# Kernel tuning notes

Measured on AMD Instinct MI355X. Metric: run time of the kernel, lower is better.

## Reference

```python
import jax, jax.numpy as jnp
import numpy as np

T = 524288          # 2**19 hash table size per level (power of 2)
F = 2               # features per table entry
NL = [16, 22, 30, 42, 58, 80, 111, 153, 212, 293, 406, 561, 775, 1071, 1481, 2046]
L_DIR = 4           # direction positional encoding freqs: 3 + 2*4*3 = 27
AABB = 3.0
PI1, PI2, PI3 = 1, 2654435761, 805459861
N_PTS = 1000000

_BITS = np.array([[(v >> k) & 1 for k in range(3)] for v in range(8)], dtype=bool)  # [8,3] corner offsets


def _linear(key, fan_in, fan_out):
    lim = 1.0 / np.sqrt(fan_in)
    kw, kb = jax.random.split(key)
    W = jax.random.uniform(kw, (fan_in, fan_out), jnp.float32, -lim, lim)
    b = jax.random.uniform(kb, (fan_out,), jnp.float32, -lim, lim)
    return W, b


def setup_inputs() -> dict:
    key = jax.random.key(0)
    ks = jax.random.split(key, 8)
    x = jax.random.normal(ks[0], (N_PTS, 3), jnp.float32)   # world-space sample points
    d = jax.random.normal(ks[1], (N_PTS, 3), jnp.float32)   # view directions
    tables = (jax.random.uniform(ks[2], (len(NL), T, F), jnp.float32) * 2 - 1) * 1e-4
    dW1, db1 = _linear(ks[3], F * len(NL), 64)
    dW2, db2 = _linear(ks[4], 64, 16)
    cW1, cb1 = _linear(ks[5], 27 + 16, 64)
    cW2, cb2 = _linear(ks[6], 64, 64)
    cW3, cb3 = _linear(ks[7], 64, 3)
    return dict(x=x, d=d, tables=tables, dW1=dW1, db1=db1, dW2=dW2, db2=db2,
                cW1=cW1, cb1=cb1, cW2=cW2, cb2=cb2, cW3=cW3, cb3=cb3)


def _hash_encode(xs, tables):
    # xs: [n,3] in [0,1]^3. Multi-resolution hash grid + trilinear interpolation.
    bits = jnp.asarray(_BITS)  # [8,3] bool
    feats = []
    for i, n in enumerate(NL):
        xn = xs * n
        fl = jnp.floor(xn)
        w = xn - fl                                   # [n,3] trilinear weights
        fl_i = fl.astype(jnp.uint32)
        ce_i = jnp.ceil(xn).astype(jnp.uint32)
        corner = jnp.where(bits[None], ce_i[:, None, :], fl_i[:, None, :])   # [n,8,3]
        # spatial hash: xor of coord * prime, mod T; T is 2**19 so uint32
        # wraparound multiply is exact mod T (bit-mask)
        h = ((corner[..., 0] * jnp.uint32(PI1))
             ^ (corner[..., 1] * jnp.uint32(PI2))
             ^ (corner[..., 2] * jnp.uint32(PI3))) & jnp.uint32(T - 1)       # [n,8]
        vals = tables[i][h]                            # [n,8,F] irregular gather
        wc = jnp.prod(jnp.where(bits[None], w[:, None, :], 1.0 - w[:, None, :]), axis=-1)  # [n,8]
        feats.append(jnp.einsum('nv,nvf->nf', wc, vals))
    return jnp.concatenate(feats, axis=1)              # [n, F*len(NL)] = [n,32]


def _pos_enc(d):
    outs = [d]
    for i in range(L_DIR):
        outs.append(jnp.sin((2.0 ** i) * d))
        outs.append(jnp.cos((2.0 ** i) * d))
    return jnp.concatenate(outs, axis=1)               # [n,27]


def reference(x, d, tables, dW1, db1, dW2, db2, cW1, cb1, cW2, cb2, cW3, cb3):
    xs = x / AABB
    mask = (jnp.abs(xs[:, 0]) < 0.5) & (jnp.abs(xs[:, 1]) < 0.5) & (jnp.abs(xs[:, 2]) < 0.5)
    xs = jnp.clip(xs + 0.5, 0.0, 1.0)                  # out-of-box rows get masked below
    feats = _hash_encode(xs, tables)
    h = jnp.maximum(feats @ dW1 + db1, 0.0) @ dW2 + db2            # [n,16] density MLP
    c_in = jnp.concatenate([h, _pos_enc(d)], axis=1)               # [n,43]
    hid = jnp.maximum(c_in @ cW1 + cb1, 0.0)
    hid = jnp.maximum(hid @ cW2 + cb2, 0.0)
    col = jax.nn.sigmoid(hid @ cW3 + cb3)                          # [n,3]
    color = jnp.where(mask[:, None], col, 0.0)
    log_sigma = jnp.where(mask, h[:, 0], -10000.0)
    return color, jnp.exp(log_sigma)
```

## Files before the change

kernel.cpp:

```cpp
#include <hip/hip_runtime.h>
#include <hip/hip_bf16.h>
#include <stdint.h>

#define TS 524288u
#define TMASK (TS - 1u)
#define QTOTAL 331757
#define NHL 11

typedef __attribute__((ext_vector_type(8))) short bf16x8;
typedef __attribute__((ext_vector_type(4))) float f32x4;

__device__ __forceinline__ short f2bf(float f) {
    union { float f; uint32_t u; } v; v.f = f;
    const uint32_t r = (v.u + 0x7fffu + ((v.u >> 16) & 1u)) >> 16;
    return (short)r;
}
__device__ __forceinline__ uint32_t cvtpk(float a, float b) {
    uint32_t r;
    asm("v_cvt_pk_bf16_f32 %0, %1, %2" : "=v"(r) : "v"(a), "v"(b));
    return r;
}
__device__ __forceinline__ short bf1(float a) { return (short)(cvtpk(a, a) & 0xffffu); }
__device__ __forceinline__ float bflo(uint32_t u) { return __uint_as_float(u << 16); }
__device__ __forceinline__ float bfhi(uint32_t u) { return __uint_as_float(u & 0xffff0000u); }
__device__ __forceinline__ uint32_t pack2(float a, float b) {
    return (uint32_t)(uint16_t)f2bf(a) | ((uint32_t)(uint16_t)f2bf(b) << 16);
}

__constant__ float c_NLf[16] = {16.f,22.f,30.f,42.f,58.f,80.f,111.f,153.f,
                                212.f,293.f,406.f,561.f,775.f,1071.f,1481.f,2046.f};
__constant__ int c_NP1[5]  = {17, 23, 31, 43, 59};
__constant__ int c_QOFF[5] = {0, 4913, 17080, 46871, 126378};

__global__ __launch_bounds__(256)
void cvt_tables_h(const float2* __restrict__ src, uint32_t* __restrict__ dst, int npairs)
{
    const int i = blockIdx.x * 256 + threadIdx.x;
    if (i >= npairs) return;
    const float2 v = src[i];
    dst[i] = pack2(v.x, v.y);
}

__global__ __launch_bounds__(256)
void build_quad(const float2* __restrict__ tbf, uint4* __restrict__ quad)
{
    const int i = blockIdx.x * 256 + threadIdx.x;
    if (i >= QTOTAL) return;
    int l, base;
    if      (i <   4913) { l = 0; base = 0;      }
    else if (i <  17080) { l = 1; base = 4913;   }
    else if (i <  46871) { l = 2; base = 17080;  }
    else if (i < 126378) { l = 3; base = 46871;  }
    else                 { l = 4; base = 126378; }
    const int np1 = c_NP1[l];
    int r = i - base;
    const int z = r % np1; r /= np1;
    const int y = r % np1;
    const int x = r / np1;
    const float2* tb = tbf + (size_t)l * TS;
    const uint32_t hx  = (uint32_t)x;
    const uint32_t hy0 = (uint32_t)y       * 2654435761u;
    const uint32_t hy1 = (uint32_t)(y + 1) * 2654435761u;
    const uint32_t hz0 = (uint32_t)z       * 805459861u;
    const uint32_t hz1 = (uint32_t)(z + 1) * 805459861u;
    const float2 a = tb[(hx ^ hy0 ^ hz0) & TMASK];
    const float2 b = tb[(hx ^ hy0 ^ hz1) & TMASK];
    const float2 c = tb[(hx ^ hy1 ^ hz0) & TMASK];
    const float2 d = tb[(hx ^ hy1 ^ hz1) & TMASK];
    uint4 q;
    q.x = pack2(a.x, a.y);
    q.y = pack2(b.x, b.y);
    q.z = pack2(c.x, c.y);
    q.w = pack2(d.x, d.y);
    quad[i] = q;
}

__device__ __forceinline__ uint32_t enc_pt(const int l, const float sx, const float sy,
                                           const float sz,
                                           const uint32_t* __restrict__ tb16h,
                                           const uint4* __restrict__ qtab)
{
    const float nf = c_NLf[l];
    const float xn0 = sx * nf, xn1 = sy * nf, xn2 = sz * nf;
    const float fl0 = floorf(xn0), fl1 = floorf(xn1), fl2 = floorf(xn2);
    const float w0 = xn0 - fl0, w1 = xn1 - fl1, w2 = xn2 - fl2;
    const uint32_t f0 = (uint32_t)fl0, f1 = (uint32_t)fl1, f2 = (uint32_t)fl2;

    float v0x,v0y,v1x,v1y,v2x,v2y,v3x,v3y,v4x,v4y,v5x,v5y,v6x,v6y,v7x,v7y;

    if (l < 5) {
        const int np1 = c_NP1[l];
        const uint4* qt = qtab + c_QOFF[l];
        const int cell = ((int)f0 * np1 + (int)f1) * np1 + (int)f2;
        const uint4 qa = qt[cell];
        const uint4 qb = qt[cell + np1 * np1];
        v0x = bflo(qa.x); v0y = bfhi(qa.x);
        v4x = bflo(qa.y); v4y = bfhi(qa.y);
        v2x = bflo(qa.z); v2y = bfhi(qa.z);
        v6x = bflo(qa.w); v6y = bfhi(qa.w);
        v1x = bflo(qb.x); v1y = bfhi(qb.x);
        v5x = bflo(qb.y); v5y = bfhi(qb.y);
        v3x = bflo(qb.z); v3y = bfhi(qb.z);
        v7x = bflo(qb.w); v7y = bfhi(qb.w);
    } else {
        const uint32_t c0 = (uint32_t)ceilf(xn0);
        const uint32_t c1 = (uint32_t)ceilf(xn1);
        const uint32_t c2 = (uint32_t)ceilf(xn2);
        const uint32_t hyf = f1 * 2654435761u, hyc = c1 * 2654435761u;
        const uint32_t hzf = f2 * 805459861u,  hzc = c2 * 805459861u;
        const uint32_t* tb = tb16h + (size_t)(l - 5) * TS;
        const uint32_t Sff = hyf ^ hzf, Scf = hyc ^ hzf;
        const uint32_t Sfc = hyf ^ hzc, Scc = hyc ^ hzc;
        uint32_t e0,e1,e2,e3,e4,e5,e6,e7;
        if ((f0 ^ c0) == 1u) {
            const uint32_t h0 = (f0 ^ Sff) & TMASK;
            const uint32_t h2 = (f0 ^ Scf) & TMASK;
            const uint32_t h4 = (f0 ^ Sfc) & TMASK;
            const uint32_t h6 = (f0 ^ Scc) & TMASK;
            const uint2 t0 = *reinterpret_cast<const uint2*>(tb + (h0 & ~1u));
            const uint2 t2 = *reinterpret_cast<const uint2*>(tb + (h2 & ~1u));
            const uint2 t4 = *reinterpret_cast<const uint2*>(tb + (h4 & ~1u));
            const uint2 t6 = *reinterpret_cast<const uint2*>(tb + (h6 & ~1u));
            e0 = (h0 & 1u) ? t0.y : t0.x;  e1 = (h0 & 1u) ? t0.x : t0.y;
            e2 = (h2 & 1u) ? t2.y : t2.x;  e3 = (h2 & 1u) ? t2.x : t2.y;
            e4 = (h4 & 1u) ? t4.y : t4.x;  e5 = (h4 & 1u) ? t4.x : t4.y;
            e6 = (h6 & 1u) ? t6.y : t6.x;  e7 = (h6 & 1u) ? t6.x : t6.y;
        } else {
            e0 = tb[(f0 ^ Sff) & TMASK];  e1 = tb[(c0 ^ Sff) & TMASK];
            e2 = tb[(f0 ^ Scf) & TMASK];  e3 = tb[(c0 ^ Scf) & TMASK];
            e4 = tb[(f0 ^ Sfc) & TMASK];  e5 = tb[(c0 ^ Sfc) & TMASK];
            e6 = tb[(f0 ^ Scc) & TMASK];  e7 = tb[(c0 ^ Scc) & TMASK];
        }
        v0x = bflo(e0); v0y = bfhi(e0); v1x = bflo(e1); v1y = bfhi(e1);
        v2x = bflo(e2); v2y = bfhi(e2); v3x = bflo(e3); v3y = bfhi(e3);
        v4x = bflo(e4); v4y = bfhi(e4); v5x = bflo(e5); v5y = bfhi(e5);
        v6x = bflo(e6); v6y = bfhi(e6); v7x = bflo(e7); v7y = bfhi(e7);
    }

    const float u0 = 1.0f - w0, u1 = 1.0f - w1, u2 = 1.0f - w2;
    float a0, a1;
    a0 = u0*u1*u2 * v0x;              a1 = u0*u1*u2 * v0y;
    a0 = fmaf(w0*u1*u2, v1x, a0);     a1 = fmaf(w0*u1*u2, v1y, a1);
    a0 = fmaf(u0*w1*u2, v2x, a0);     a1 = fmaf(u0*w1*u2, v2y, a1);
    a0 = fmaf(w0*w1*u2, v3x, a0);     a1 = fmaf(w0*w1*u2, v3y, a1);
    a0 = fmaf(u0*u1*w2, v4x, a0);     a1 = fmaf(u0*u1*w2, v4y, a1);
    a0 = fmaf(w0*u1*w2, v5x, a0);     a1 = fmaf(w0*u1*w2, v5y, a1);
    a0 = fmaf(u0*w1*w2, v6x, a0);     a1 = fmaf(u0*w1*w2, v6y, a1);
    a0 = fmaf(w0*w1*w2, v7x, a0);     a1 = fmaf(w0*w1*w2, v7y, a1);

    return cvtpk(a0, a1);
}

__global__ __launch_bounds__(256)
void ngp_encode_lm(const float* __restrict__ xg, const uint32_t* __restrict__ tb16h,
                   const uint4* __restrict__ qtab, uint32_t* __restrict__ feats_lm,
                   const int n, const unsigned tiles)
{
    const unsigned b = blockIdx.x;
    const int l = (int)(b / tiles);
    const int p = (int)(b - (unsigned)l * tiles) * 256 + threadIdx.x;
    if (p >= n) return;

    float sx = xg[3*p+0] / 3.0f, sy = xg[3*p+1] / 3.0f, sz = xg[3*p+2] / 3.0f;
    if (!((fabsf(sx) < 0.5f) && (fabsf(sy) < 0.5f) && (fabsf(sz) < 0.5f))) {
        feats_lm[(size_t)l * n + p] = 0u;
        return;
    }
    sx = fminf(fmaxf(sx + 0.5f, 0.0f), 1.0f);
    sy = fminf(fmaxf(sy + 0.5f, 0.0f), 1.0f);
    sz = fminf(fmaxf(sz + 0.5f, 0.0f), 1.0f);
    feats_lm[(size_t)l * n + p] = enc_pt(l, sx, sy, sz, tb16h, qtab);
}

__global__ __launch_bounds__(256)
void ngp_encode_f32(const float* __restrict__ xg, const float2* __restrict__ tbf,
                    uint32_t* __restrict__ feats_lm, const int n, const unsigned tiles)
{
    const unsigned b = blockIdx.x;
    const int l = (int)(b / tiles);
    const int p = (int)(b - (unsigned)l * tiles) * 256 + threadIdx.x;
    if (p >= n) return;
    float sx = xg[3*p+0] / 3.0f, sy = xg[3*p+1] / 3.0f, sz = xg[3*p+2] / 3.0f;
    if (!((fabsf(sx) < 0.5f) && (fabsf(sy) < 0.5f) && (fabsf(sz) < 0.5f))) {
        feats_lm[(size_t)l * n + p] = 0u;
        return;
    }
    sx = fminf(fmaxf(sx + 0.5f, 0.0f), 1.0f);
    sy = fminf(fmaxf(sy + 0.5f, 0.0f), 1.0f);
    sz = fminf(fmaxf(sz + 0.5f, 0.0f), 1.0f);
    const float nf = c_NLf[l];
    const float xn0 = sx*nf, xn1 = sy*nf, xn2 = sz*nf;
    const float fl0 = floorf(xn0), fl1 = floorf(xn1), fl2 = floorf(xn2);
    const float w0 = xn0-fl0, w1 = xn1-fl1, w2 = xn2-fl2;
    const uint32_t f0=(uint32_t)fl0, f1=(uint32_t)fl1, f2=(uint32_t)fl2;
    const uint32_t c0=(uint32_t)ceilf(xn0), c1=(uint32_t)ceilf(xn1), c2=(uint32_t)ceilf(xn2);
    const uint32_t hyf = f1*2654435761u, hyc = c1*2654435761u;
    const uint32_t hzf = f2*805459861u,  hzc = c2*805459861u;
    const float2* tb = tbf + (size_t)l * TS;
    const float2 e0 = tb[(f0^hyf^hzf)&TMASK], e1 = tb[(c0^hyf^hzf)&TMASK];
    const float2 e2 = tb[(f0^hyc^hzf)&TMASK], e3 = tb[(c0^hyc^hzf)&TMASK];
    const float2 e4 = tb[(f0^hyf^hzc)&TMASK], e5 = tb[(c0^hyf^hzc)&TMASK];
    const float2 e6 = tb[(f0^hyc^hzc)&TMASK], e7 = tb[(c0^hyc^hzc)&TMASK];
    const float u0 = 1.0f-w0, u1 = 1.0f-w1, u2 = 1.0f-w2;
    float a0, a1;
    a0 = u0*u1*u2 * e0.x;             a1 = u0*u1*u2 * e0.y;
    a0 = fmaf(w0*u1*u2, e1.x, a0);    a1 = fmaf(w0*u1*u2, e1.y, a1);
    a0 = fmaf(u0*w1*u2, e2.x, a0);    a1 = fmaf(u0*w1*u2, e2.y, a1);
    a0 = fmaf(w0*w1*u2, e3.x, a0);    a1 = fmaf(w0*w1*u2, e3.y, a1);
    a0 = fmaf(u0*u1*w2, e4.x, a0);    a1 = fmaf(u0*u1*w2, e4.y, a1);
    a0 = fmaf(w0*u1*w2, e5.x, a0);    a1 = fmaf(w0*u1*w2, e5.y, a1);
    a0 = fmaf(u0*w1*w2, e6.x, a0);    a1 = fmaf(u0*w1*w2, e6.y, a1);
    a0 = fmaf(w0*w1*w2, e7.x, a0);    a1 = fmaf(w0*w1*w2, e7.y, a1);
    feats_lm[(size_t)l * n + p] = pack2(a0, a1);
}

#define ACT_STRIDE 72

__global__ __launch_bounds__(256)
void ngp_mlp_mfma(const float* __restrict__ xg, const float* __restrict__ dg,
                  const uint32_t* __restrict__ feats_lm,
                  const float* __restrict__ dW1, const float* __restrict__ db1,
                  const float* __restrict__ dW2, const float* __restrict__ db2,
                  const float* __restrict__ cW1, const float* __restrict__ cb1,
                  const float* __restrict__ cW2, const float* __restrict__ cb2,
                  const float* __restrict__ cW3, const float* __restrict__ cb3,
                  float* __restrict__ out, int n)
{
    __shared__ __align__(16) short w1[2048];
    __shared__ __align__(16) short w2[1024];
    __shared__ __align__(16) short w3[4096];
    __shared__ __align__(16) short w4[4096];
    __shared__ __align__(16) short w5[1024];
    __shared__ __align__(16) float b1[64];
    __shared__ __align__(16) float b2[16];
    __shared__ __align__(16) float b3[64];
    __shared__ __align__(16) float b4[64];
    __shared__ __align__(16) float b5[16];
    __shared__ __align__(16) short act[4][16*ACT_STRIDE];

    const int tid = threadIdx.x;

    for (int i2 = tid; i2 < 4*16*ACT_STRIDE/2; i2 += 256)
        reinterpret_cast<uint32_t*>(act)[i2] = 0u;

    for (int i2 = tid; i2 < 2048; i2 += 256) {
        const int jb = i2 >> 9, lane = (i2 >> 3) & 63, e = i2 & 7;
        const int j = jb*16 + (lane & 15), k = ((lane >> 4) << 3) + e;
        w1[i2] = f2bf(dW1[k*64 + j]);
    }
    for (int i2 = tid; i2 < 1024; i2 += 256) {
        const int kb = i2 >> 9, lane = (i2 >> 3) & 63, e = i2 & 7;
        const int j = lane & 15, k = kb*32 + ((lane >> 4) << 3) + e;
        w2[i2] = f2bf(dW2[k*16 + j]);
    }
    for (int i2 = tid; i2 < 4096; i2 += 256) {
        const int jb = i2 >> 10, kb = (i2 >> 9) & 1, lane = (i2 >> 3) & 63, e = i2 & 7;
        const int j = jb*16 + (lane & 15), k = kb*32 + ((lane >> 4) << 3) + e;
        w3[i2] = (k < 43) ? f2bf(cW1[k*64 + j]) : (short)0;
        w4[i2] = f2bf(cW2[k*64 + j]);
    }
    for (int i2 = tid; i2 < 1024; i2 += 256) {
        const int kb = i2 >> 9, lane = (i2 >> 3) & 63, e = i2 & 7;
        const int j = lane & 15, k = kb*32 + ((lane >> 4) << 3) + e;
        w5[i2] = (j < 3) ? f2bf(cW3[k*3 + j]) : (short)0;
    }
    if (tid < 64) { b1[tid] = db1[tid]; b3[tid] = cb1[tid]; b4[tid] = cb2[tid]; }
    if (tid < 16) { b2[tid] = db2[tid]; b5[tid] = (tid < 3) ? cb3[tid] : 0.0f; }
    __syncthreads();

    const int wv = tid >> 6, lane = tid & 63;
    const int p16 = lane & 15, quad = lane >> 4;
    short* buf = &act[wv][0];

    const int ntiles = (n + 63) >> 6;
    for (int t = blockIdx.x; t < ntiles; t += gridDim.x) {
        const int pp_raw = t*64 + wv*16 + p16;
        const int pp = (pp_raw < n) ? pp_raw : (n - 1);
        const bool valid = (pp_raw < n);

        const float mx = xg[3*pp+0] / 3.0f, my = xg[3*pp+1] / 3.0f, mz = xg[3*pp+2] / 3.0f;
        const bool inside = (fabsf(mx) < 0.5f) && (fabsf(my) < 0.5f) && (fabsf(mz) < 0.5f);

        union { int4 i; bf16x8 v; } bu;
        bu.i.x = (int)feats_lm[(size_t)(4*quad+0)*n + pp];
        bu.i.y = (int)feats_lm[(size_t)(4*quad+1)*n + pp];
        bu.i.z = (int)feats_lm[(size_t)(4*quad+2)*n + pp];
        bu.i.w = (int)feats_lm[(size_t)(4*quad+3)*n + pp];
        const bf16x8 bA = bu.v;
        #pragma unroll
        for (int jb = 0; jb < 4; ++jb) {
            const int j0 = jb*16 + quad*4;
            f32x4 acc = *reinterpret_cast<const f32x4*>(&b1[j0]);
            const bf16x8 aF = *reinterpret_cast<const bf16x8*>(&w1[(jb*64 + lane)*8]);
            acc = __builtin_amdgcn_mfma_f32_16x16x32_bf16(aF, bA, acc, 0, 0, 0);
            uint2 s;
            s.x = cvtpk(fmaxf(acc[0], 0.f), fmaxf(acc[1], 0.f));
            s.y = cvtpk(fmaxf(acc[2], 0.f), fmaxf(acc[3], 0.f));
            *reinterpret_cast<uint2*>(&buf[p16*ACT_STRIDE + j0]) = s;
        }

        {
            const bf16x8 bF0 = *reinterpret_cast<const bf16x8*>(&buf[p16*ACT_STRIDE + quad*8]);
            const bf16x8 bF1 = *reinterpret_cast<const bf16x8*>(&buf[p16*ACT_STRIDE + 32 + quad*8]);
            f32x4 acc2 = *reinterpret_cast<const f32x4*>(&b2[quad*4]);
            acc2 = __builtin_amdgcn_mfma_f32_16x16x32_bf16(
                *reinterpret_cast<const bf16x8*>(&w2[lane*8]), bF0, acc2, 0, 0, 0);
            acc2 = __builtin_amdgcn_mfma_f32_16x16x32_bf16(
                *reinterpret_cast<const bf16x8*>(&w2[(64 + lane)*8]), bF1, acc2, 0, 0, 0);
            if (quad == 0 && valid)
                out[(size_t)3*n + pp] = inside ? __expf(acc2[0]) : 0.0f;
            uint2 s;
            s.x = cvtpk(acc2[0], acc2[1]);
            s.y = cvtpk(acc2[2], acc2[3]);
            *reinterpret_cast<uint2*>(&buf[p16*ACT_STRIDE + quad*4]) = s;
        }
        if (quad < 3) {
            const float v = dg[3*pp + quad];
            buf[p16*ACT_STRIDE + 16 + quad] = bf1(v);
            float arg = v;
            #pragma unroll
            for (int f = 0; f < 4; ++f) {
                buf[p16*ACT_STRIDE + 19 + 6*f + quad] = bf1(__sinf(arg));
                buf[p16*ACT_STRIDE + 22 + 6*f + quad] = bf1(__cosf(arg));
                arg += arg;
            }
        }

        {
            const bf16x8 bF0 = *reinterpret_cast<const bf16x8*>(&buf[p16*ACT_STRIDE + quad*8]);
            const bf16x8 bF1 = *reinterpret_cast<const bf16x8*>(&buf[p16*ACT_STRIDE + 32 + quad*8]);
            #pragma unroll
            for (int jb = 0; jb < 4; ++jb) {
                const int j0 = jb*16 + quad*4;
                f32x4 acc = *reinterpret_cast<const f32x4*>(&b3[j0]);
                acc = __builtin_amdgcn_mfma_f32_16x16x32_bf16(
                    *reinterpret_cast<const bf16x8*>(&w3[((jb*2 + 0)*64 + lane)*8]), bF0, acc, 0, 0, 0);
                acc = __builtin_amdgcn_mfma_f32_16x16x32_bf16(
                    *reinterpret_cast<const bf16x8*>(&w3[((jb*2 + 1)*64 + lane)*8]), bF1, acc, 0, 0, 0);
                uint2 s;
                s.x = cvtpk(fmaxf(acc[0], 0.f), fmaxf(acc[1], 0.f));
                s.y = cvtpk(fmaxf(acc[2], 0.f), fmaxf(acc[3], 0.f));
                *reinterpret_cast<uint2*>(&buf[p16*ACT_STRIDE + j0]) = s;
            }
        }

        {
            const bf16x8 bF0 = *reinterpret_cast<const bf16x8*>(&buf[p16*ACT_STRIDE + quad*8]);
            const bf16x8 bF1 = *reinterpret_cast<const bf16x8*>(&buf[p16*ACT_STRIDE + 32 + quad*8]);
            #pragma unroll
            for (int jb = 0; jb < 4; ++jb) {
                const int j0 = jb*16 + quad*4;
                f32x4 acc = *reinterpret_cast<const f32x4*>(&b4[j0]);
                acc = __builtin_amdgcn_mfma_f32_16x16x32_bf16(
                    *reinterpret_cast<const bf16x8*>(&w4[((jb*2 + 0)*64 + lane)*8]), bF0, acc, 0, 0, 0);
                acc = __builtin_amdgcn_mfma_f32_16x16x32_bf16(
                    *reinterpret_cast<const bf16x8*>(&w4[((jb*2 + 1)*64 + lane)*8]), bF1, acc, 0, 0, 0);
                uint2 s;
                s.x = cvtpk(fmaxf(acc[0], 0.f), fmaxf(acc[1], 0.f));
                s.y = cvtpk(fmaxf(acc[2], 0.f), fmaxf(acc[3], 0.f));
                *reinterpret_cast<uint2*>(&buf[p16*ACT_STRIDE + j0]) = s;
            }
        }

        {
            const bf16x8 bF0 = *reinterpret_cast<const bf16x8*>(&buf[p16*ACT_STRIDE + quad*8]);
            const bf16x8 bF1 = *reinterpret_cast<const bf16x8*>(&buf[p16*ACT_STRIDE + 32 + quad*8]);
            f32x4 acc5 = *reinterpret_cast<const f32x4*>(&b5[quad*4]);
            acc5 = __builtin_amdgcn_mfma_f32_16x16x32_bf16(
                *reinterpret_cast<const bf16x8*>(&w5[lane*8]), bF0, acc5, 0, 0, 0);
            acc5 = __builtin_amdgcn_mfma_f32_16x16x32_bf16(
                *reinterpret_cast<const bf16x8*>(&w5[(64 + lane)*8]), bF1, acc5, 0, 0, 0);
            if (quad == 0 && valid) {
                #pragma unroll
                for (int r = 0; r < 3; ++r) {
                    const float s = 1.0f / (1.0f + __expf(-acc5[r]));
                    out[3*(size_t)pp + r] = inside ? s : 0.0f;
                }
            }
        }
    }
}

extern "C" void kernel_launch(void* const* d_in, const int* in_sizes, int n_in,
                              void* d_out, int out_size, void* d_ws, size_t ws_size,
                              hipStream_t stream)
{
    const float* x   = (const float*)d_in[0];
    const float* d   = (const float*)d_in[1];
    const float* tb  = (const float*)d_in[2];
    const float* dW1 = (const float*)d_in[3];
    const float* db1 = (const float*)d_in[4];
    const float* dW2 = (const float*)d_in[5];
    const float* db2 = (const float*)d_in[6];
    const float* cW1 = (const float*)d_in[7];
    const float* cb1 = (const float*)d_in[8];
    const float* cW2 = (const float*)d_in[9];
    const float* cb2 = (const float*)d_in[10];
    const float* cW3 = (const float*)d_in[11];
    const float* cb3 = (const float*)d_in[12];
    float* out = (float*)d_out;

    const int n = in_sizes[0] / 3;

    size_t off = 0;
    uint32_t* feats_lm = (uint32_t*)d_ws;                 off += (size_t)n * 16 * 4;
    uint32_t* tb16h    = (uint32_t*)((char*)d_ws + off);  off += (size_t)NHL * TS * 4;
    uint4*    quadbuf  = (uint4*)((char*)d_ws + off);     off += (size_t)QTOTAL * 16;
    const bool planA = (ws_size >= off);

    const unsigned tiles = (unsigned)((n + 255) / 256);

    if (planA) {
        {
            const int npairs = NHL * (int)TS;
            hipLaunchKernelGGL(cvt_tables_h, dim3((npairs + 255) / 256), dim3(256), 0, stream,
                               (const float2*)tb + 5 * (size_t)TS, tb16h, npairs);
        }
        hipLaunchKernelGGL(build_quad, dim3((QTOTAL + 255) / 256), dim3(256), 0, stream,
                           (const float2*)tb, quadbuf);
        hipLaunchKernelGGL(ngp_encode_lm, dim3(tiles * 16), dim3(256), 0, stream,
                           x, tb16h, quadbuf, feats_lm, n, tiles);
    } else {
        hipLaunchKernelGGL(ngp_encode_f32, dim3(tiles * 16), dim3(256), 0, stream,
                           x, (const float2*)tb, feats_lm, n, tiles);
    }
    {
        const int ntiles = (n + 63) >> 6;
        const int nblk = (ntiles < 1024) ? ntiles : 1024;
        dim3 block(256), grid(nblk);
        hipLaunchKernelGGL(ngp_mlp_mfma, grid, block, 0, stream,
                           x, d, feats_lm, dW1, db1, dW2, db2,
                           cW1, cb1, cW2, cb2, cW3, cb3, out, n);
    }
}
```

Baseline: 378.9 us.

## Split encode into quad and hash kernels; prefetch next tile in MLP

```diff
diff --git a/kernel.cpp b/kernel.cpp
--- a/kernel.cpp
+++ b/kernel.cpp
@@ -75,101 +75,138 @@
     quad[i] = q;
 }
 
-__device__ __forceinline__ uint32_t enc_pt(const int l, const float sx, const float sy,
-                                           const float sz,
-                                           const uint32_t* __restrict__ tb16h,
-                                           const uint4* __restrict__ qtab)
-{
-    const float nf = c_NLf[l];
+__global__ __launch_bounds__(256)
+void ngp_encode_quad(const float* __restrict__ xg, const uint4* __restrict__ qtab,
+                     uint32_t* __restrict__ feats_lm, const int n)
+{
+    const int p = blockIdx.x * 256 + threadIdx.x;
+    if (p >= n) return;
+
+    float sx = xg[3*p+0] / 3.0f, sy = xg[3*p+1] / 3.0f, sz = xg[3*p+2] / 3.0f;
+    if (!((fabsf(sx) < 0.5f) && (fabsf(sy) < 0.5f) && (fabsf(sz) < 0.5f))) {
+        #pragma unroll
+        for (int l = 0; l < 5; ++l) feats_lm[(size_t)l * n + p] = 0u;
+        return;
+    }
+    sx = fminf(fmaxf(sx + 0.5f, 0.0f), 1.0f);
+    sy = fminf(fmaxf(sy + 0.5f, 0.0f), 1.0f);
+    sz = fminf(fmaxf(sz + 0.5f, 0.0f), 1.0f);
+
+    const float nfs[5]  = {16.f, 22.f, 30.f, 42.f, 58.f};
+    const int   np1s[5] = {17, 23, 31, 43, 59};
+    const int   qoff[5] = {0, 4913, 17080, 46871, 126378};
+
+    #pragma unroll
+    for (int l = 0; l < 5; ++l) {
+        const float nf = nfs[l];
+        const float xn0 = sx * nf, xn1 = sy * nf, xn2 = sz * nf;
+        const float fl0 = floorf(xn0), fl1 = floorf(xn1), fl2 = floorf(xn2);
+        const float w0 = xn0 - fl0, w1 = xn1 - fl1, w2 = xn2 - fl2;
+        const int np1 = np1s[l];
+        const uint4* qt = qtab + qoff[l];
+        const int cell = ((int)fl0 * np1 + (int)fl1) * np1 + (int)fl2;
+        const uint4 qa = qt[cell];
+        const uint4 qb = qt[cell + np1 * np1];
+        const float v0x = bflo(qa.x), v0y = bfhi(qa.x);
+        const float v4x = bflo(qa.y), v4y = bfhi(qa.y);
+        const float v2x = bflo(qa.z), v2y = bfhi(qa.z);
+        const float v6x = bflo(qa.w), v6y = bfhi(qa.w);
+        const float v1x = bflo(qb.x), v1y = bfhi(qb.x);
+        const float v5x = bflo(qb.y), v5y = bfhi(qb.y);
+        const float v3x = bflo(qb.z), v3y = bfhi(qb.z);
+        const float v7x = bflo(qb.w), v7y = bfhi(qb.w);
+
+        const float u0 = 1.0f - w0, u1 = 1.0f - w1, u2 = 1.0f - w2;
+        float a0, a1;
+        a0 = u0*u1*u2 * v0x;              a1 = u0*u1*u2 * v0y;
+        a0 = fmaf(w0*u1*u2, v1x, a0);     a1 = fmaf(w0*u1*u2, v1y, a1);
+        a0 = fmaf(u0*w1*u2, v2x, a0);     a1 = fmaf(u0*w1*u2, v2y, a1);
+        a0 = fmaf(w0*w1*u2, v3x, a0);     a1 = fmaf(w0*w1*u2, v3y, a1);
+        a0 = fmaf(u0*u1*w2, v4x, a0);     a1 = fmaf(u0*u1*w2, v4y, a1);
+        a0 = fmaf(w0*u1*w2, v5x, a0);     a1 = fmaf(w0*u1*w2, v5y, a1);
+        a0 = fmaf(u0*w1*w2, v6x, a0);     a1 = fmaf(u0*w1*w2, v6y, a1);
+        a0 = fmaf(w0*w1*w2, v7x, a0);     a1 = fmaf(w0*w1*w2, v7y, a1);
+        feats_lm[(size_t)l * n + p] = cvtpk(a0, a1);
+    }
+}
+
+__device__ __forceinline__ uint32_t enc_hash(const float nf, const uint32_t* __restrict__ tb,
+                                             const float sx, const float sy, const float sz)
+{
     const float xn0 = sx * nf, xn1 = sy * nf, xn2 = sz * nf;
     const float fl0 = floorf(xn0), fl1 = floorf(xn1), fl2 = floorf(xn2);
     const float w0 = xn0 - fl0, w1 = xn1 - fl1, w2 = xn2 - fl2;
     const uint32_t f0 = (uint32_t)fl0, f1 = (uint32_t)fl1, f2 = (uint32_t)fl2;
-
-    float v0x,v0y,v1x,v1y,v2x,v2y,v3x,v3y,v4x,v4y,v5x,v5y,v6x,v6y,v7x,v7y;
-
-    if (l < 5) {
-        const int np1 = c_NP1[l];
-        const uint4* qt = qtab + c_QOFF[l];
-        const int cell = ((int)f0 * np1 + (int)f1) * np1 + (int)f2;
-        const uint4 qa = qt[cell];
-        const uint4 qb = qt[cell + np1 * np1];
-        v0x = bflo(qa.x); v0y = bfhi(qa.x);
-        v4x = bflo(qa.y); v4y = bfhi(qa.y);
-        v2x = bflo(qa.z); v2y = bfhi(qa.z);
-        v6x = bflo(qa.w); v6y = bfhi(qa.w);
-        v1x = bflo(qb.x); v1y = bfhi(qb.x);
-        v5x = bflo(qb.y); v5y = bfhi(qb.y);
-        v3x = bflo(qb.z); v3y = bfhi(qb.z);
-        v7x = bflo(qb.w); v7y = bfhi(qb.w);
-    } else {
-        const uint32_t c0 = (uint32_t)ceilf(xn0);
-        const uint32_t c1 = (uint32_t)ceilf(xn1);
-        const uint32_t c2 = (uint32_t)ceilf(xn2);
-        const uint32_t hyf = f1 * 2654435761u, hyc = c1 * 2654435761u;
-        const uint32_t hzf = f2 * 805459861u,  hzc = c2 * 805459861u;
-        const uint32_t* tb = tb16h + (size_t)(l - 5) * TS;
-        const uint32_t Sff = hyf ^ hzf, Scf = hyc ^ hzf;
-        const uint32_t Sfc = hyf ^ hzc, Scc = hyc ^ hzc;
-        uint32_t e0,e1,e2,e3,e4,e5,e6,e7;
-        if ((f0 ^ c0) == 1u) {
-            const uint32_t h0 = (f0 ^ Sff) & TMASK;
-            const uint32_t h2 = (f0 ^ Scf) & TMASK;
-            const uint32_t h4 = (f0 ^ Sfc) & TMASK;
-            const uint32_t h6 = (f0 ^ Scc) & TMASK;
-            const uint2 t0 = *reinterpret_cast<const uint2*>(tb + (h0 & ~1u));
-            const uint2 t2 = *reinterpret_cast<const uint2*>(tb + (h2 & ~1u));
-            const uint2 t4 = *reinterpret_cast<const uint2*>(tb + (h4 & ~1u));
-            const uint2 t6 = *reinterpret_cast<const uint2*>(tb + (h6 & ~1u));
-            e0 = (h0 & 1u) ? t0.y : t0.x;  e1 = (h0 & 1u) ? t0.x : t0.y;
-            e2 = (h2 & 1u) ? t2.y : t2.x;  e3 = (h2 & 1u) ? t2.x : t2.y;
-            e4 = (h4 & 1u) ? t4.y : t4.x;  e5 = (h4 & 1u) ? t4.x : t4.y;
-            e6 = (h6 & 1u) ? t6.y : t6.x;  e7 = (h6 & 1u) ? t6.x : t6.y;
-        } else {
-            e0 = tb[(f0 ^ Sff) & TMASK];  e1 = tb[(c0 ^ Sff) & TMASK];
-            e2 = tb[(f0 ^ Scf) & TMASK];  e3 = tb[(c0 ^ Scf) & TMASK];
-            e4 = tb[(f0 ^ Sfc) & TMASK];  e5 = tb[(c0 ^ Sfc) & TMASK];
-            e6 = tb[(f0 ^ Scc) & TMASK];  e7 = tb[(c0 ^ Scc) & TMASK];
-        }
-        v0x = bflo(e0); v0y = bfhi(e0); v1x = bflo(e1); v1y = bfhi(e1);
-        v2x = bflo(e2); v2y = bfhi(e2); v3x = bflo(e3); v3y = bfhi(e3);
-        v4x = bflo(e4); v4y = bfhi(e4); v5x = bflo(e5); v5y = bfhi(e5);
-        v6x = bflo(e6); v6y = bfhi(e6); v7x = bflo(e7); v7y = bfhi(e7);
+    const uint32_t c0 = (uint32_t)ceilf(xn0);
+    const uint32_t c1 = (uint32_t)ceilf(xn1);
+    const uint32_t c2 = (uint32_t)ceilf(xn2);
+
+    const uint32_t hyf = f1 * 2654435761u, hyc = c1 * 2654435761u;
+    const uint32_t hzf = f2 * 805459861u,  hzc = c2 * 805459861u;
+    const uint32_t S0 = hyf ^ hzf, S1 = hyc ^ hzf, S2 = hyf ^ hzc, S3 = hyc ^ hzc;
+
+    const uint32_t h0 = (f0 ^ S0) & TMASK;
+    const uint32_t h1 = (f0 ^ S1) & TMASK;
+    const uint32_t h2 = (f0 ^ S2) & TMASK;
+    const uint32_t h3 = (f0 ^ S3) & TMASK;
+    const uint2 p0 = *reinterpret_cast<const uint2*>(tb + (h0 & ~1u));
+    const uint2 p1 = *reinterpret_cast<const uint2*>(tb + (h1 & ~1u));
+    const uint2 p2 = *reinterpret_cast<const uint2*>(tb + (h2 & ~1u));
+    const uint2 p3 = *reinterpret_cast<const uint2*>(tb + (h3 & ~1u));
+    const uint32_t e0 = (h0 & 1u) ? p0.y : p0.x;
+    const uint32_t e2 = (h1 & 1u) ? p1.y : p1.x;
+    const uint32_t e4 = (h2 & 1u) ? p2.y : p2.x;
+    const uint32_t e6 = (h3 & 1u) ? p3.y : p3.x;
+    uint32_t e1 = (h0 & 1u) ? p0.x : p0.y;
+    uint32_t e3 = (h1 & 1u) ? p1.x : p1.y;
+    uint32_t e5 = (h2 & 1u) ? p2.x : p2.y;
+    uint32_t e7 = (h3 & 1u) ? p3.x : p3.y;
+    if (f0 & 1u) {
+        e1 = tb[(c0 ^ S0) & TMASK];
+        e3 = tb[(c0 ^ S1) & TMASK];
+        e5 = tb[(c0 ^ S2) & TMASK];
+        e7 = tb[(c0 ^ S3) & TMASK];
     }
 
     const float u0 = 1.0f - w0, u1 = 1.0f - w1, u2 = 1.0f - w2;
     float a0, a1;
-    a0 = u0*u1*u2 * v0x;              a1 = u0*u1*u2 * v0y;
-    a0 = fmaf(w0*u1*u2, v1x, a0);     a1 = fmaf(w0*u1*u2, v1y, a1);
-    a0 = fmaf(u0*w1*u2, v2x, a0);     a1 = fmaf(u0*w1*u2, v2y, a1);
-    a0 = fmaf(w0*w1*u2, v3x, a0);     a1 = fmaf(w0*w1*u2, v3y, a1);
-    a0 = fmaf(u0*u1*w2, v4x, a0);     a1 = fmaf(u0*u1*w2, v4y, a1);
-    a0 = fmaf(w0*u1*w2, v5x, a0);     a1 = fmaf(w0*u1*w2, v5y, a1);
-    a0 = fmaf(u0*w1*w2, v6x, a0);     a1 = fmaf(u0*w1*w2, v6y, a1);
-    a0 = fmaf(w0*w1*w2, v7x, a0);     a1 = fmaf(w0*w1*w2, v7y, a1);
+    a0 = u0*u1*u2 * bflo(e0);              a1 = u0*u1*u2 * bfhi(e0);
+    a0 = fmaf(w0*u1*u2, bflo(e1), a0);     a1 = fmaf(w0*u1*u2, bfhi(e1), a1);
+    a0 = fmaf(u0*w1*u2, bflo(e2), a0);     a1 = fmaf(u0*w1*u2, bfhi(e2), a1);
+    a0 = fmaf(w0*w1*u2, bflo(e3), a0);     a1 = fmaf(w0*w1*u2, bfhi(e3), a1);
+    a0 = fmaf(u0*u1*w2, bflo(e4), a0);     a1 = fmaf(u0*u1*w2, bfhi(e4), a1);
+    a0 = fmaf(w0*u1*w2, bflo(e5), a0);     a1 = fmaf(w0*u1*w2, bfhi(e5), a1);
+    a0 = fmaf(u0*w1*w2, bflo(e6), a0);     a1 = fmaf(u0*w1*w2, bfhi(e6), a1);
+    a0 = fmaf(w0*w1*w2, bflo(e7), a0);     a1 = fmaf(w0*w1*w2, bfhi(e7), a1);
 
     return cvtpk(a0, a1);
 }
 
 __global__ __launch_bounds__(256)
-void ngp_encode_lm(const float* __restrict__ xg, const uint32_t* __restrict__ tb16h,
-                   const uint4* __restrict__ qtab, uint32_t* __restrict__ feats_lm,
-                   const int n, const unsigned tiles)
+void ngp_encode_hash(const float* __restrict__ xg, const uint32_t* __restrict__ tb16h,
+                     uint32_t* __restrict__ feats_lm, const int n, const unsigned tiles2)
 {
     const unsigned b = blockIdx.x;
-    const int l = (int)(b / tiles);
-    const int p = (int)(b - (unsigned)l * tiles) * 256 + threadIdx.x;
-    if (p >= n) return;
-
-    float sx = xg[3*p+0] / 3.0f, sy = xg[3*p+1] / 3.0f, sz = xg[3*p+2] / 3.0f;
-    if (!((fabsf(sx) < 0.5f) && (fabsf(sy) < 0.5f) && (fabsf(sz) < 0.5f))) {
-        feats_lm[(size_t)l * n + p] = 0u;
-        return;
-    }
-    sx = fminf(fmaxf(sx + 0.5f, 0.0f), 1.0f);
-    sy = fminf(fmaxf(sy + 0.5f, 0.0f), 1.0f);
-    sz = fminf(fmaxf(sz + 0.5f, 0.0f), 1.0f);
-    feats_lm[(size_t)l * n + p] = enc_pt(l, sx, sy, sz, tb16h, qtab);
+    const int l5 = (int)(b / tiles2);
+    const int p0 = (int)(b - (unsigned)l5 * tiles2) * 512 + threadIdx.x;
+    const float nf = c_NLf[l5 + 5];
+    const uint32_t* tb = tb16h + (size_t)l5 * TS;
+    uint32_t* fl = feats_lm + (size_t)(l5 + 5) * n;
+
+    #pragma unroll
+    for (int s = 0; s < 2; ++s) {
+        const int p = p0 + s * 256;
+        if (p >= n) continue;
+        float sx = xg[3*p+0] / 3.0f, sy = xg[3*p+1] / 3.0f, sz = xg[3*p+2] / 3.0f;
+        if (!((fabsf(sx) < 0.5f) && (fabsf(sy) < 0.5f) && (fabsf(sz) < 0.5f))) {
+            fl[p] = 0u;
+            continue;
+        }
+        sx = fminf(fmaxf(sx + 0.5f, 0.0f), 1.0f);
+        sy = fminf(fmaxf(sy + 0.5f, 0.0f), 1.0f);
+        sz = fminf(fmaxf(sz + 0.5f, 0.0f), 1.0f);
+        fl[p] = enc_hash(nf, tb, sx, sy, sz);
+    }
 }
 
 __global__ __launch_bounds__(256)
@@ -270,22 +307,47 @@
 
     const int wv = tid >> 6, lane = tid & 63;
     const int p16 = lane & 15, quad = lane >> 4;
+    const int dc = (quad < 3) ? quad : 0;
     short* buf = &act[wv][0];
 
     const int ntiles = (n + 63) >> 6;
-    for (int t = blockIdx.x; t < ntiles; t += gridDim.x) {
-        const int pp_raw = t*64 + wv*16 + p16;
-        const int pp = (pp_raw < n) ? pp_raw : (n - 1);
-        const bool valid = (pp_raw < n);
-
-        const float mx = xg[3*pp+0] / 3.0f, my = xg[3*pp+1] / 3.0f, mz = xg[3*pp+2] / 3.0f;
-        const bool inside = (fabsf(mx) < 0.5f) && (fabsf(my) < 0.5f) && (fabsf(mz) < 0.5f);
+    int t = blockIdx.x;
+    if (t >= ntiles) return;
+
+    int pp_n; bool valid_n;
+    uint32_t fn0, fn1, fn2, fn3;
+    float xn0, xn1, xn2, dn;
+
+    auto issue = [&](int tt) {
+        const int pr = tt*64 + wv*16 + p16;
+        valid_n = (pr < n);
+        pp_n = valid_n ? pr : (n - 1);
+        fn0 = feats_lm[(size_t)(4*quad+0)*n + pp_n];
+        fn1 = feats_lm[(size_t)(4*quad+1)*n + pp_n];
+        fn2 = feats_lm[(size_t)(4*quad+2)*n + pp_n];
+        fn3 = feats_lm[(size_t)(4*quad+3)*n + pp_n];
+        xn0 = xg[3*pp_n+0];
+        xn1 = xg[3*pp_n+1];
+        xn2 = xg[3*pp_n+2];
+        dn  = dg[3*pp_n + dc];
+    };
+
+    issue(t);
+    while (t < ntiles) {
+        const int pp = pp_n;
+        const bool valid = valid_n;
+        const uint32_t fc0 = fn0, fc1 = fn1, fc2 = fn2, fc3 = fn3;
+        const float xc0 = xn0, xc1 = xn1, xc2 = xn2;
+        const float dv = dn;
+
+        const int t2 = t + gridDim.x;
+        if (t2 < ntiles) issue(t2);
+
+        const bool inside = (fabsf(xc0 / 3.0f) < 0.5f) && (fabsf(xc1 / 3.0f) < 0.5f)
+                         && (fabsf(xc2 / 3.0f) < 0.5f);
 
         union { int4 i; bf16x8 v; } bu;
-        bu.i.x = (int)feats_lm[(size_t)(4*quad+0)*n + pp];
-        bu.i.y = (int)feats_lm[(size_t)(4*quad+1)*n + pp];
-        bu.i.z = (int)feats_lm[(size_t)(4*quad+2)*n + pp];
-        bu.i.w = (int)feats_lm[(size_t)(4*quad+3)*n + pp];
+        bu.i.x = (int)fc0; bu.i.y = (int)fc1; bu.i.z = (int)fc2; bu.i.w = (int)fc3;
         const bf16x8 bA = bu.v;
         #pragma unroll
         for (int jb = 0; jb < 4; ++jb) {
@@ -315,9 +377,8 @@
             *reinterpret_cast<uint2*>(&buf[p16*ACT_STRIDE + quad*4]) = s;
         }
         if (quad < 3) {
-            const float v = dg[3*pp + quad];
-            buf[p16*ACT_STRIDE + 16 + quad] = bf1(v);
-            float arg = v;
+            buf[p16*ACT_STRIDE + 16 + quad] = bf1(dv);
+            float arg = dv;
             #pragma unroll
             for (int f = 0; f < 4; ++f) {
                 buf[p16*ACT_STRIDE + 19 + 6*f + quad] = bf1(__sinf(arg));
@@ -378,6 +439,7 @@
                 }
             }
         }
+        t = t2;
     }
 }
 
@@ -408,8 +470,6 @@
     uint4*    quadbuf  = (uint4*)((char*)d_ws + off);     off += (size_t)QTOTAL * 16;
     const bool planA = (ws_size >= off);
 
-    const unsigned tiles = (unsigned)((n + 255) / 256);
-
     if (planA) {
         {
             const int npairs = NHL * (int)TS;
@@ -418,9 +478,18 @@
         }
         hipLaunchKernelGGL(build_quad, dim3((QTOTAL + 255) / 256), dim3(256), 0, stream,
                            (const float2*)tb, quadbuf);
-        hipLaunchKernelGGL(ngp_encode_lm, dim3(tiles * 16), dim3(256), 0, stream,
-                           x, tb16h, quadbuf, feats_lm, n, tiles);
+        {
+            const unsigned tiles = (unsigned)((n + 255) / 256);
+            hipLaunchKernelGGL(ngp_encode_quad, dim3(tiles), dim3(256), 0, stream,
+                               x, quadbuf, feats_lm, n);
+        }
+        {
+            const unsigned tiles2 = (unsigned)((n + 511) / 512);
+            hipLaunchKernelGGL(ngp_encode_hash, dim3(tiles2 * NHL), dim3(256), 0, stream,
+                               x, tb16h, feats_lm, n, tiles2);
+        }
     } else {
+        const unsigned tiles = (unsigned)((n + 255) / 256);
         hipLaunchKernelGGL(ngp_encode_f32, dim3(tiles * 16), dim3(256), 0, stream,
                            x, (const float2*)tb, feats_lm, n, tiles);
     }
```

Result: slower. 424.0 us (+11.9%).

## Keep MLP weights in registers and prefetch next tile's inputs in MLP kernel

Applied to the files above, without the earlier changes.

```diff
diff --git a/kernel.cpp b/kernel.cpp
--- a/kernel.cpp
+++ b/kernel.cpp
@@ -216,7 +216,7 @@
 
 #define ACT_STRIDE 72
 
-__global__ __launch_bounds__(256)
+__global__ __launch_bounds__(256, 2)
 void ngp_mlp_mfma(const float* __restrict__ xg, const float* __restrict__ dg,
                   const uint32_t* __restrict__ feats_lm,
                   const float* __restrict__ dW1, const float* __restrict__ db1,
@@ -270,29 +270,75 @@
 
     const int wv = tid >> 6, lane = tid & 63;
     const int p16 = lane & 15, quad = lane >> 4;
+    const int dc = (quad < 3) ? quad : 0;
     short* buf = &act[wv][0];
 
+    bf16x8 A1[4], A2[2], A3[8], A4[8], A5[2];
+    #pragma unroll
+    for (int jb = 0; jb < 4; ++jb) A1[jb] = *reinterpret_cast<const bf16x8*>(&w1[(jb*64 + lane)*8]);
+    #pragma unroll
+    for (int kb = 0; kb < 2; ++kb) A2[kb] = *reinterpret_cast<const bf16x8*>(&w2[(kb*64 + lane)*8]);
+    #pragma unroll
+    for (int i = 0; i < 8; ++i) {
+        A3[i] = *reinterpret_cast<const bf16x8*>(&w3[(i*64 + lane)*8]);
+        A4[i] = *reinterpret_cast<const bf16x8*>(&w4[(i*64 + lane)*8]);
+    }
+    #pragma unroll
+    for (int kb = 0; kb < 2; ++kb) A5[kb] = *reinterpret_cast<const bf16x8*>(&w5[(kb*64 + lane)*8]);
+    f32x4 B1[4], B3[4], B4[4];
+    #pragma unroll
+    for (int jb = 0; jb < 4; ++jb) {
+        B1[jb] = *reinterpret_cast<const f32x4*>(&b1[jb*16 + quad*4]);
+        B3[jb] = *reinterpret_cast<const f32x4*>(&b3[jb*16 + quad*4]);
+        B4[jb] = *reinterpret_cast<const f32x4*>(&b4[jb*16 + quad*4]);
+    }
+    const f32x4 B2v = *reinterpret_cast<const f32x4*>(&b2[quad*4]);
+    const f32x4 B5v = *reinterpret_cast<const f32x4*>(&b5[quad*4]);
+
     const int ntiles = (n + 63) >> 6;
-    for (int t = blockIdx.x; t < ntiles; t += gridDim.x) {
-        const int pp_raw = t*64 + wv*16 + p16;
-        const int pp = (pp_raw < n) ? pp_raw : (n - 1);
-        const bool valid = (pp_raw < n);
-
-        const float mx = xg[3*pp+0] / 3.0f, my = xg[3*pp+1] / 3.0f, mz = xg[3*pp+2] / 3.0f;
-        const bool inside = (fabsf(mx) < 0.5f) && (fabsf(my) < 0.5f) && (fabsf(mz) < 0.5f);
+    int t = blockIdx.x;
+    if (t >= ntiles) return;
+
+    int pp_n; bool valid_n;
+    uint32_t fn0, fn1, fn2, fn3;
+    float xn0, xn1, xn2, dn;
+
+    auto issue = [&](int tt) {
+        const int pr = tt*64 + wv*16 + p16;
+        valid_n = (pr < n);
+        pp_n = valid_n ? pr : (n - 1);
+        fn0 = feats_lm[(size_t)(4*quad+0)*n + pp_n];
+        fn1 = feats_lm[(size_t)(4*quad+1)*n + pp_n];
+        fn2 = feats_lm[(size_t)(4*quad+2)*n + pp_n];
+        fn3 = feats_lm[(size_t)(4*quad+3)*n + pp_n];
+        xn0 = xg[3*pp_n+0];
+        xn1 = xg[3*pp_n+1];
+        xn2 = xg[3*pp_n+2];
+        dn  = dg[3*pp_n + dc];
+    };
+
+    issue(t);
+    while (t < ntiles) {
+        const int pp = pp_n;
+        const bool valid = valid_n;
+        const uint32_t fc0 = fn0, fc1 = fn1, fc2 = fn2, fc3 = fn3;
+        const float xc0 = xn0, xc1 = xn1, xc2 = xn2;
+        const float dv = dn;
+
+        const int t2 = t + gridDim.x;
+        if (t2 < ntiles) issue(t2);
+
+        const bool inside = (fabsf(xc0 / 3.0f) < 0.5f) && (fabsf(xc1 / 3.0f) < 0.5f)
+                         && (fabsf(xc2 / 3.0f) < 0.5f);
 
         union { int4 i; bf16x8 v; } bu;
-        bu.i.x = (int)feats_lm[(size_t)(4*quad+0)*n + pp];
-        bu.i.y = (int)feats_lm[(size_t)(4*quad+1)*n + pp];
-        bu.i.z = (int)feats_lm[(size_t)(4*quad+2)*n + pp];
-        bu.i.w = (int)feats_lm[(size_t)(4*quad+3)*n + pp];
+        bu.i.x = (int)fc0; bu.i.y = (int)fc1; bu.i.z = (int)fc2; bu.i.w = (int)fc3;
         const bf16x8 bA = bu.v;
         #pragma unroll
         for (int jb = 0; jb < 4; ++jb) {
             const int j0 = jb*16 + quad*4;
-            f32x4 acc = *reinterpret_cast<const f32x4*>(&b1[j0]);
-            const bf16x8 aF = *reinterpret_cast<const bf16x8*>(&w1[(jb*64 + lane)*8]);
-            acc = __builtin_amdgcn_mfma_f32_16x16x32_bf16(aF, bA, acc, 0, 0, 0);
+            f32x4 acc = B1[jb];
+            acc = __builtin_amdgcn_mfma_f32_16x16x32_bf16(A1[jb], bA, acc, 0, 0, 0);
             uint2 s;
             s.x = cvtpk(fmaxf(acc[0], 0.f), fmaxf(acc[1], 0.f));
             s.y = cvtpk(fmaxf(acc[2], 0.f), fmaxf(acc[3], 0.f));
@@ -302,11 +348,9 @@
         {
             const bf16x8 bF0 = *reinterpret_cast<const bf16x8*>(&buf[p16*ACT_STRIDE + quad*8]);
             const bf16x8 bF1 = *reinterpret_cast<const bf16x8*>(&buf[p16*ACT_STRIDE + 32 + quad*8]);
-            f32x4 acc2 = *reinterpret_cast<const f32x4*>(&b2[quad*4]);
-            acc2 = __builtin_amdgcn_mfma_f32_16x16x32_bf16(
-                *reinterpret_cast<const bf16x8*>(&w2[lane*8]), bF0, acc2, 0, 0, 0);
-            acc2 = __builtin_amdgcn_mfma_f32_16x16x32_bf16(
-                *reinterpret_cast<const bf16x8*>(&w2[(64 + lane)*8]), bF1, acc2, 0, 0, 0);
+            f32x4 acc2 = B2v;
+            acc2 = __builtin_amdgcn_mfma_f32_16x16x32_bf16(A2[0], bF0, acc2, 0, 0, 0);
+            acc2 = __builtin_amdgcn_mfma_f32_16x16x32_bf16(A2[1], bF1, acc2, 0, 0, 0);
             if (quad == 0 && valid)
                 out[(size_t)3*n + pp] = inside ? __expf(acc2[0]) : 0.0f;
             uint2 s;
@@ -315,9 +359,8 @@
             *reinterpret_cast<uint2*>(&buf[p16*ACT_STRIDE + quad*4]) = s;
         }
         if (quad < 3) {
-            const float v = dg[3*pp + quad];
-            buf[p16*ACT_STRIDE + 16 + quad] = bf1(v);
-            float arg = v;
+            buf[p16*ACT_STRIDE + 16 + quad] = bf1(dv);
+            float arg = dv;
             #pragma unroll
             for (int f = 0; f < 4; ++f) {
                 buf[p16*ACT_STRIDE + 19 + 6*f + quad] = bf1(__sinf(arg));
@@ -332,11 +375,9 @@
             #pragma unroll
             for (int jb = 0; jb < 4; ++jb) {
                 const int j0 = jb*16 + quad*4;
-                f32x4 acc = *reinterpret_cast<const f32x4*>(&b3[j0]);
-                acc = __builtin_amdgcn_mfma_f32_16x16x32_bf16(
-                    *reinterpret_cast<const bf16x8*>(&w3[((jb*2 + 0)*64 + lane)*8]), bF0, acc, 0, 0, 0);
-                acc = __builtin_amdgcn_mfma_f32_16x16x32_bf16(
-                    *reinterpret_cast<const bf16x8*>(&w3[((jb*2 + 1)*64 + lane)*8]), bF1, acc, 0, 0, 0);
+                f32x4 acc = B3[jb];
+                acc = __builtin_amdgcn_mfma_f32_16x16x32_bf16(A3[jb*2 + 0], bF0, acc, 0, 0, 0);
+                acc = __builtin_amdgcn_mfma_f32_16x16x32_bf16(A3[jb*2 + 1], bF1, acc, 0, 0, 0);
                 uint2 s;
                 s.x = cvtpk(fmaxf(acc[0], 0.f), fmaxf(acc[1], 0.f));
                 s.y = cvtpk(fmaxf(acc[2], 0.f), fmaxf(acc[3], 0.f));
@@ -350,11 +391,9 @@
             #pragma unroll
             for (int jb = 0; jb < 4; ++jb) {
                 const int j0 = jb*16 + quad*4;
-                f32x4 acc = *reinterpret_cast<const f32x4*>(&b4[j0]);
-                acc = __builtin_amdgcn_mfma_f32_16x16x32_bf16(
-                    *reinterpret_cast<const bf16x8*>(&w4[((jb*2 + 0)*64 + lane)*8]), bF0, acc, 0, 0, 0);
-                acc = __builtin_amdgcn_mfma_f32_16x16x32_bf16(
-                    *reinterpret_cast<const bf16x8*>(&w4[((jb*2 + 1)*64 + lane)*8]), bF1, acc, 0, 0, 0);
+                f32x4 acc = B4[jb];
+                acc = __builtin_amdgcn_mfma_f32_16x16x32_bf16(A4[jb*2 + 0], bF0, acc, 0, 0, 0);
+                acc = __builtin_amdgcn_mfma_f32_16x16x32_bf16(A4[jb*2 + 1], bF1, acc, 0, 0, 0);
                 uint2 s;
                 s.x = cvtpk(fmaxf(acc[0], 0.f), fmaxf(acc[1], 0.f));
                 s.y = cvtpk(fmaxf(acc[2], 0.f), fmaxf(acc[3], 0.f));
@@ -365,11 +404,9 @@
         {
             const bf16x8 bF0 = *reinterpret_cast<const bf16x8*>(&buf[p16*ACT_STRIDE + quad*8]);
             const bf16x8 bF1 = *reinterpret_cast<const bf16x8*>(&buf[p16*ACT_STRIDE + 32 + quad*8]);
-            f32x4 acc5 = *reinterpret_cast<const f32x4*>(&b5[quad*4]);
-            acc5 = __builtin_amdgcn_mfma_f32_16x16x32_bf16(
-                *reinterpret_cast<const bf16x8*>(&w5[lane*8]), bF0, acc5, 0, 0, 0);
-            acc5 = __builtin_amdgcn_mfma_f32_16x16x32_bf16(
-                *reinterpret_cast<const bf16x8*>(&w5[(64 + lane)*8]), bF1, acc5, 0, 0, 0);
+            f32x4 acc5 = B5v;
+            acc5 = __builtin_amdgcn_mfma_f32_16x16x32_bf16(A5[0], bF0, acc5, 0, 0, 0);
+            acc5 = __builtin_amdgcn_mfma_f32_16x16x32_bf16(A5[1], bF1, acc5, 0, 0, 0);
             if (quad == 0 && valid) {
                 #pragma unroll
                 for (int r = 0; r < 3; ++r) {
@@ -378,6 +415,7 @@
                 }
             }
         }
+        t = t2;
     }
 }
 
@@ -426,7 +464,7 @@
     }
     {
         const int ntiles = (n + 63) >> 6;
-        const int nblk = (ntiles < 1024) ? ntiles : 1024;
+        const int nblk = (ntiles < 512) ? ntiles : 512;
         dim3 block(256), grid(nblk);
         hipLaunchKernelGGL(ngp_mlp_mfma, grid, block, 0, stream,
                            x, d, feats_lm, dW1, db1, dW2, db2,
```

Result: faster. 367.5 us (-3.0%).
